# Optimization experiments

Measured on AMD Instinct MI355X. Metric: run time of the kernel, lower is better.

## Reference

```python
import jax, jax.numpy as jnp
import numpy as np

D_MODEL = 1024
NUM_HEADS = 16
HEAD_DIM = D_MODEL // NUM_HEADS
B, S = 2, 2048


def setup_inputs() -> dict:
    key = jax.random.key(0)
    ks = jax.random.split(key, 8)
    scale = 1.0 / np.sqrt(D_MODEL)
    inp = {
        "query": jax.random.normal(ks[0], (B, S, D_MODEL), jnp.float32),
        "key": jax.random.normal(ks[1], (B, S, D_MODEL), jnp.float32),
        "value": jax.random.normal(ks[2], (B, S, D_MODEL), jnp.float32),
        # causal mask, broadcastable over batch and heads
        "mask": jnp.tril(jnp.ones((S, S), dtype=bool))[None, None, :, :],
        # torch nn.Linear weights: y = x @ W.T (+ b)
        "Wq": jax.random.normal(ks[3], (D_MODEL, D_MODEL), jnp.float32) * scale,
        "Wk": jax.random.normal(ks[4], (D_MODEL, D_MODEL), jnp.float32) * scale,
        "Wv": jax.random.normal(ks[5], (D_MODEL, D_MODEL), jnp.float32) * scale,
        "Wo": jax.random.normal(ks[6], (D_MODEL, D_MODEL), jnp.float32) * scale,
        "bo": jax.random.normal(ks[7], (D_MODEL,), jnp.float32) * scale,
    }
    return inp


def _split_heads(x):
    b, s, _ = x.shape
    return x.reshape(b, s, NUM_HEADS, HEAD_DIM).transpose(0, 2, 1, 3)  # [B,H,S,Dh]


def reference(query, key, value, mask, Wq, Wk, Wv, Wo, bo):
    q = _split_heads(query @ Wq.T)
    k = _split_heads(key @ Wk.T)
    v = _split_heads(value @ Wv.T)
    scores = jnp.einsum("bhqd,bhkd->bhqk", q, k) / jnp.sqrt(jnp.float32(HEAD_DIM))
    scores = jnp.where(mask, scores, jnp.float32(-jnp.inf))
    attn = jax.nn.softmax(scores, axis=-1)
    out = jnp.einsum("bhqk,bhkd->bhqd", attn, v)  # [B,H,S,Dh]
    out = out.transpose(0, 2, 1, 3).reshape(query.shape[0], q.shape[2], D_MODEL)
    return out @ Wo.T + bo
```

## Files before the change

kernel.cpp:

```cpp
#include <hip/hip_runtime.h>
#include <hip/hip_bf16.h>

#define DM   1024
#define NH   16
#define HD   64
#define SEQ  2048
#define BATCH 2
#define MTOT (BATCH*SEQ)

typedef unsigned short u16;
typedef __attribute__((ext_vector_type(8))) short bf16x8;
typedef __attribute__((ext_vector_type(4))) float f32x4;

#define SC2F 0.1803368801111464f

__device__ __forceinline__ float bf2f(u16 h) {
  union { unsigned int i; float f; } u; u.i = ((unsigned int)h) << 16; return u.f;
}
__device__ __forceinline__ u16 f2bf(float f) {
  union { float f; unsigned int i; } u; u.f = f;
  unsigned int r = u.i + 0x7fffu + ((u.i >> 16) & 1u);
  return (u16)(r >> 16);
}
__device__ __forceinline__ unsigned int pk2(float lo, float hi) {
  union { float f; unsigned int u; } a, b; a.f = lo; b.f = hi;
  return ((a.u + 0x8000u) >> 16) | ((b.u + 0x8000u) & 0xFFFF0000u);
}
__device__ __forceinline__ unsigned int cvtpk(float lo, float hi) {
  unsigned int r;
  asm("v_cvt_pk_bf16_f32 %0, %1, %2" : "=v"(r) : "v"(lo), "v"(hi));
  return r;
}

__device__ __forceinline__ uint4 load8_bf16(const void* base, size_t elemOff, bool isf32) {
  if (!isf32) return *(const uint4*)((const u16*)base + elemOff);
  const float* f = (const float*)base + elemOff;
  f32x4 a = *(const f32x4*)f;
  f32x4 b = *(const f32x4*)(f + 4);
  union { u16 h[8]; uint4 v; } r;
  r.h[0]=f2bf(a[0]); r.h[1]=f2bf(a[1]); r.h[2]=f2bf(a[2]); r.h[3]=f2bf(a[3]);
  r.h[4]=f2bf(b[0]); r.h[5]=f2bf(b[1]); r.h[6]=f2bf(b[2]); r.h[7]=f2bf(b[3]);
  return r.v;
}

__global__ __launch_bounds__(256) void prep(
    const void* __restrict__ q, const void* __restrict__ k, const void* __restrict__ v,
    const void* __restrict__ wq, const void* __restrict__ wk, const void* __restrict__ wv,
    const void* __restrict__ wo, const void* __restrict__ bo,
    u16* __restrict__ Xq, u16* __restrict__ Xk, u16* __restrict__ Xv,
    u16* __restrict__ Wqb, u16* __restrict__ Wkb, u16* __restrict__ Wvb, u16* __restrict__ Wob,
    float* __restrict__ biasf, int* __restrict__ flag_out)
{
  const int tid = threadIdx.x;
  __shared__ int cnts[4];
  {
    const u16* qs = (const u16*)q;
    int e0 = (qs[tid*2]   >> 7) & 0xFF;
    int e1 = (qs[tid*2+1] >> 7) & 0xFF;
    int c = ((e0 >= 0x6E && e0 <= 0x8F) ? 1 : 0) + ((e1 >= 0x6E && e1 <= 0x8F) ? 1 : 0);
    c += __shfl_xor(c, 1);  c += __shfl_xor(c, 2);  c += __shfl_xor(c, 4);
    c += __shfl_xor(c, 8);  c += __shfl_xor(c, 16); c += __shfl_xor(c, 32);
    if ((tid & 63) == 0) cnts[tid >> 6] = c;
  }
  __syncthreads();
  const bool isf32 = (cnts[0] + cnts[1] + cnts[2] + cnts[3]) < 400;

  const int z = blockIdx.z;
  if (z == 7) {
    if (blockIdx.x == 0) {
      if (tid == 0) *flag_out = isf32 ? 0 : 1;
      for (int i = tid; i < DM; i += 256)
        biasf[i] = isf32 ? ((const float*)bo)[i] : bf2f(((const u16*)bo)[i]);
    }
    return;
  }
  const void* src; u16* dst; size_t n;
  switch (z) {
    case 0: src=q;  dst=Xq;  n=(size_t)MTOT*DM; break;
    case 1: src=k;  dst=Xk;  n=(size_t)MTOT*DM; break;
    case 2: src=v;  dst=Xv;  n=(size_t)MTOT*DM; break;
    case 3: src=wq; dst=Wqb; n=(size_t)DM*DM;   break;
    case 4: src=wk; dst=Wkb; n=(size_t)DM*DM;   break;
    case 5: src=wv; dst=Wvb; n=(size_t)DM*DM;   break;
    default: src=wo; dst=Wob; n=(size_t)DM*DM;  break;
  }
  const size_t stride = (size_t)gridDim.x * 256 * 8;
  for (size_t i = ((size_t)blockIdx.x * 256 + tid) * 8; i < n; i += stride)
    *(uint4*)(dst + i) = load8_bf16(src, i, isf32);
}

__device__ __forceinline__ void gld16(const u16* g, u16* l) {
  __builtin_amdgcn_global_load_lds(
      (const __attribute__((address_space(1))) void*)g,
      (__attribute__((address_space(3))) void*)l, 16, 0, 0);
}

__global__ __launch_bounds__(256) void gemm_qkv(
    const u16* __restrict__ X0, const u16* __restrict__ X1, const u16* __restrict__ X2,
    const u16* __restrict__ W0, const u16* __restrict__ W1, const u16* __restrict__ W2,
    u16* __restrict__ F0, u16* __restrict__ F1, u16* __restrict__ F2)
{
  __shared__ __align__(16) u16 smem[24576];
  u16* const A0 = smem;
  u16* const A1 = smem + 4096;
  u16* const A2 = smem + 8192;
  u16* const B0 = smem + 12288;
  u16* const B1 = smem + 16384;
  u16* const B2 = smem + 20480;

  const int zz = blockIdx.z;
  const u16* X = (zz==0) ? X0 : ((zz==1) ? X1 : X2);
  const u16* W = (zz==0) ? W0 : ((zz==1) ? W1 : W2);
  u16* outF    = (zz==0) ? F0 : ((zz==1) ? F1 : F2);

  const int tid = threadIdx.x;
  const int wave = tid >> 6, lane = tid & 63, quad = lane >> 4, l16 = lane & 15;
  const int wr = wave >> 1, wc = wave & 1;
  const int m0 = blockIdx.x * 128, n0 = blockIdx.y * 128;

  const int sg = ((lane & 3) ^ ((lane >> 3) & 3)) * 8;
  const int rS = wave*32 + (lane >> 2);
  const u16* gA0 = X + (size_t)(m0 + rS)*DM + sg;
  const u16* gA1 = X + (size_t)(m0 + rS + 16)*DM + sg;
  const u16* gB0 = W + (size_t)(n0 + rS)*DM + sg;
  const u16* gB1 = W + (size_t)(n0 + rS + 16)*DM + sg;
  const int so = wave*1024;

  const int xslot8 = (quad ^ ((l16 >> 1) & 3)) * 8;

  f32x4 acc[4][4];
#pragma unroll
  for (int i = 0; i < 4; i++)
#pragma unroll
    for (int j = 0; j < 4; j++) { acc[i][j][0]=0.f; acc[i][j][1]=0.f; acc[i][j][2]=0.f; acc[i][j][3]=0.f; }

  gld16(gA0, A0 + so);
  gld16(gA1, A0 + so + 512);
  gld16(gB0, B0 + so);
  gld16(gB1, B0 + so + 512);
  gld16(gA0 + 32, A1 + so);
  gld16(gA1 + 32, A1 + so + 512);
  gld16(gB0 + 32, B1 + so);
  gld16(gB1 + 32, B1 + so + 512);
  asm volatile("" ::: "memory");

  int cur = 0;
  for (int k0 = 0; k0 < DM; k0 += 32) {
    u16* const Ab = (cur == 0) ? A0 : ((cur == 1) ? A1 : A2);
    u16* const Bb = (cur == 0) ? B0 : ((cur == 1) ? B1 : B2);
    const int nxt = (cur == 2) ? 0 : cur + 1;
    const int nx2 = (nxt == 2) ? 0 : nxt + 1;
    if (k0 + 64 < DM) {
      u16* const An = (nx2 == 0) ? A0 : ((nx2 == 1) ? A1 : A2);
      u16* const Bn = (nx2 == 0) ? B0 : ((nx2 == 1) ? B1 : B2);
      gld16(gA0 + k0 + 64, An + so);
      gld16(gA1 + k0 + 64, An + so + 512);
      gld16(gB0 + k0 + 64, Bn + so);
      gld16(gB1 + k0 + 64, Bn + so + 512);
      asm volatile("s_waitcnt vmcnt(8)" ::: "memory");
    } else if (k0 + 32 < DM) {
      asm volatile("s_waitcnt vmcnt(4)" ::: "memory");
    } else {
      asm volatile("s_waitcnt vmcnt(0)" ::: "memory");
    }
    __builtin_amdgcn_s_barrier();
    asm volatile("" ::: "memory");

    bf16x8 af[4], bfr[4];
#pragma unroll
    for (int fr = 0; fr < 4; fr++)
      af[fr] = *(const bf16x8*)&Ab[(wr*64 + fr*16 + l16)*32 + xslot8];
#pragma unroll
    for (int fc = 0; fc < 4; fc++)
      bfr[fc] = *(const bf16x8*)&Bb[(wc*64 + fc*16 + l16)*32 + xslot8];
#pragma unroll
    for (int fr = 0; fr < 4; fr++)
#pragma unroll
      for (int fc = 0; fc < 4; fc++)
        acc[fr][fc] = __builtin_amdgcn_mfma_f32_16x16x32_bf16(af[fr], bfr[fc], acc[fr][fc], 0, 0, 0);

    asm volatile("" ::: "memory");
    __builtin_amdgcn_s_barrier();
    asm volatile("" ::: "memory");
    cur = nxt;
  }

  if (zz == 2) {
    u16* const Ts = smem;
    const int bb = m0 >> 11;
    const int s0 = m0 & (SEQ-1);
#pragma unroll
    for (int p = 0; p < 2; p++) {
      __syncthreads();
      if (wc == p) {
#pragma unroll
        for (int fr = 0; fr < 4; fr++) {
#pragma unroll
          for (int fc = 0; fc < 4; fc++) {
            const int dl = fc*16 + l16;
            const int sb = wr*64 + fr*16 + quad*4;
            const int slot = (sb >> 3) ^ (dl & 15);
            u16* rowp = &Ts[dl*128 + slot*8 + (sb & 7)];
            *(unsigned int*)(rowp)     = pk2(acc[fr][fc][0], acc[fr][fc][1]);
            *(unsigned int*)(rowp + 2) = pk2(acc[fr][fc][2], acc[fr][fc][3]);
          }
        }
      }
      __syncthreads();
      const int dl2 = tid >> 2, ch4 = tid & 3;
      const int hh = (n0 + p*64) >> 6;
      u16* dst = outF + ((size_t)(bb*NH + hh)*HD + dl2)*SEQ + s0 + ch4*32;
#pragma unroll
      for (int j = 0; j < 4; j++) {
        const int c  = ch4*4 + j;
        const int lo = (c >> 2)*32 + (c & 3)*4;
        const int hi = lo + 16;
        uint2 lo2 = *(const uint2*)&Ts[dl2*128 + (((lo >> 3) ^ (dl2 & 15))*8) + (lo & 7)];
        uint2 hi2 = *(const uint2*)&Ts[dl2*128 + (((hi >> 3) ^ (dl2 & 15))*8) + (hi & 7)];
        uint4 o; o.x = lo2.x; o.y = lo2.y; o.z = hi2.x; o.w = hi2.y;
        *(uint4*)&dst[j*8] = o;
      }
    }
    return;
  }

#pragma unroll
  for (int fr = 0; fr < 4; fr++) {
#pragma unroll
    for (int rr = 0; rr < 4; rr++) {
      const int m = m0 + wr*64 + fr*16 + quad*4 + rr;
#pragma unroll
      for (int fc = 0; fc < 4; fc++) {
        const int n = n0 + wc*64 + fc*16 + l16;
        float vv = acc[fr][fc][rr];
        if (zz == 0) vv *= SC2F;
        const int b = m >> 11, s = m & (SEQ-1), h = n >> 6, d = n & (HD-1);
        outF[((size_t)(b*NH + h)*SEQ + s)*HD + d] = f2bf(vv);
      }
    }
  }
}

__global__ __launch_bounds__(256) void gemm_out(
    const u16* __restrict__ X, const u16* __restrict__ W,
    const float* __restrict__ biasf, void* __restrict__ outP,
    const int* __restrict__ dflag)
{
  __shared__ __align__(16) u16 smem[18432];
  u16* const A0 = smem;
  u16* const A1 = smem + 4096;
  u16* const A2 = smem + 8192;
  u16* const B0 = smem + 12288;
  u16* const B1 = smem + 14336;
  u16* const B2 = smem + 16384;

  const int tid = threadIdx.x;
  const int wave = tid >> 6, lane = tid & 63, quad = lane >> 4, l16 = lane & 15;
  const int wr = wave >> 1, wc = wave & 1;
  const int m0 = blockIdx.x * 128, n0 = blockIdx.y * 64;

  const int sg = ((lane & 3) ^ ((lane >> 3) & 3)) * 8;
  const int rA = wave*32 + (lane >> 2);
  const int rB = wave*16 + (lane >> 2);
  const u16* gA0 = X + (size_t)(m0 + rA)*DM + sg;
  const u16* gA1 = X + (size_t)(m0 + rA + 16)*DM + sg;
  const u16* gB0 = W + (size_t)(n0 + rB)*DM + sg;
  const int soA = wave*1024, soB = wave*512;

  const int xslot8 = (quad ^ ((l16 >> 1) & 3)) * 8;

  f32x4 acc[4][2];
#pragma unroll
  for (int i = 0; i < 4; i++)
#pragma unroll
    for (int j = 0; j < 2; j++) { acc[i][j][0]=0.f; acc[i][j][1]=0.f; acc[i][j][2]=0.f; acc[i][j][3]=0.f; }

  gld16(gA0, A0 + soA);
  gld16(gA1, A0 + soA + 512);
  gld16(gB0, B0 + soB);
  gld16(gA0 + 32, A1 + soA);
  gld16(gA1 + 32, A1 + soA + 512);
  gld16(gB0 + 32, B1 + soB);
  asm volatile("" ::: "memory");

  int cur = 0;
  for (int k0 = 0; k0 < DM; k0 += 32) {
    u16* const Ab = (cur == 0) ? A0 : ((cur == 1) ? A1 : A2);
    u16* const Bb = (cur == 0) ? B0 : ((cur == 1) ? B1 : B2);
    const int nxt = (cur == 2) ? 0 : cur + 1;
    const int nx2 = (nxt == 2) ? 0 : nxt + 1;
    if (k0 + 64 < DM) {
      u16* const An = (nx2 == 0) ? A0 : ((nx2 == 1) ? A1 : A2);
      u16* const Bn = (nx2 == 0) ? B0 : ((nx2 == 1) ? B1 : B2);
      gld16(gA0 + k0 + 64, An + soA);
      gld16(gA1 + k0 + 64, An + soA + 512);
      gld16(gB0 + k0 + 64, Bn + soB);
      asm volatile("s_waitcnt vmcnt(6)" ::: "memory");
    } else if (k0 + 32 < DM) {
      asm volatile("s_waitcnt vmcnt(3)" ::: "memory");
    } else {
      asm volatile("s_waitcnt vmcnt(0)" ::: "memory");
    }
    __builtin_amdgcn_s_barrier();
    asm volatile("" ::: "memory");

    bf16x8 af[4], bfr[2];
#pragma unroll
    for (int fr = 0; fr < 4; fr++)
      af[fr] = *(const bf16x8*)&Ab[(wr*64 + fr*16 + l16)*32 + xslot8];
#pragma unroll
    for (int fc = 0; fc < 2; fc++)
      bfr[fc] = *(const bf16x8*)&Bb[(wc*32 + fc*16 + l16)*32 + xslot8];
#pragma unroll
    for (int fr = 0; fr < 4; fr++)
#pragma unroll
      for (int fc = 0; fc < 2; fc++)
        acc[fr][fc] = __builtin_amdgcn_mfma_f32_16x16x32_bf16(af[fr], bfr[fc], acc[fr][fc], 0, 0, 0);

    asm volatile("" ::: "memory");
    __builtin_amdgcn_s_barrier();
    asm volatile("" ::: "memory");
    cur = nxt;
  }

  const bool isf32 = (*dflag == 0);
#pragma unroll
  for (int fr = 0; fr < 4; fr++) {
#pragma unroll
    for (int rr = 0; rr < 4; rr++) {
      const int m = m0 + wr*64 + fr*16 + quad*4 + rr;
#pragma unroll
      for (int fc = 0; fc < 2; fc++) {
        const int n = n0 + wc*32 + fc*16 + l16;
        float vv = acc[fr][fc][rr] + biasf[n];
        if (isf32) ((float*)outP)[(size_t)m*DM + n] = vv;
        else       ((u16*)outP)[(size_t)m*DM + n]   = f2bf(vv);
      }
    }
  }
}

__global__ __launch_bounds__(256) void attn_mfma(
    const u16* __restrict__ Qb, const u16* __restrict__ Kb,
    const u16* __restrict__ Vtb,
    u16* __restrict__ aO)
{
  __shared__ u16 Ks[2][64*64];
  __shared__ u16 Vs[2][64*64];

  const int bh = blockIdx.x;
  const int py = blockIdx.y;
  int qt;
  if      (py < 8)  qt = 31 - py;
  else if (py < 16) qt = py - 8;
  else if (py < 24) qt = 39 - py;
  else              qt = py - 16;

  const u16* Qp = Qb  + (size_t)bh * SEQ * HD;
  const u16* Kp = Kb  + (size_t)bh * SEQ * HD;
  const u16* Vp = Vtb + (size_t)bh * HD * SEQ;

  const int tid  = threadIdx.x;
  const int wave = tid >> 6, lane = tid & 63, quad = lane >> 4, l16 = lane & 15;

  const int i0 = wave*128 + lane, i1 = i0 + 64;
  const int r0 = i0 >> 3, c0 = (i0 & 7) ^ (r0 & 7);
  const int r1 = i1 >> 3, c1 = (i1 & 7) ^ (r1 & 7);
  const int kq_off0 = r0*HD + c0*8;
  const int kq_off1 = r1*HD + c1*8;
  const int v_off0  = r0*SEQ + c0*8;
  const int v_off1  = r1*SEQ + c1*8;

  const int l7 = l16 & 7;
  const int ql = wave*16 + l16;
  const int so = wave*1024;

  const int khi = qt + 1;
  const int qg = qt*64 + ql;

  const u16* qrow = Qp + (size_t)qg * HD;
  const bf16x8 bq0 = *(const bf16x8*)(qrow + quad*8);
  const bf16x8 bq1 = *(const bf16x8*)(qrow + 32 + quad*8);

  f32x4 O[4];
#pragma unroll
  for (int u = 0; u < 4; u++) { O[u][0]=0.f; O[u][1]=0.f; O[u][2]=0.f; O[u][3]=0.f; }
  float mi = -3.0e38f;
  f32x4 lv = {0.f, 0.f, 0.f, 0.f};

  gld16(Kp + kq_off0, &Ks[0][so]);
  gld16(Kp + kq_off1, &Ks[0][so + 512]);
  gld16(Vp + v_off0, &Vs[0][so]);
  gld16(Vp + v_off1, &Vs[0][so + 512]);
  asm volatile("" ::: "memory");

  for (int kt = 0; kt < khi; kt++) {
    const int cb = kt & 1;
    const u16* kb = &Ks[cb][0];
    const u16* vb = &Vs[cb][0];
    if (kt + 1 < khi) {
      u16* kn = &Ks[cb ^ 1][so];
      u16* vn = &Vs[cb ^ 1][so];
      gld16(Kp + (kt+1)*(64*HD) + kq_off0, kn);
      gld16(Kp + (kt+1)*(64*HD) + kq_off1, kn + 512);
      gld16(Vp + (kt+1)*64 + v_off0, vn);
      gld16(Vp + (kt+1)*64 + v_off1, vn + 512);
      asm volatile("s_waitcnt vmcnt(4)" ::: "memory");
    } else {
      asm volatile("s_waitcnt vmcnt(0)" ::: "memory");
    }
    __builtin_amdgcn_s_barrier();
    asm volatile("" ::: "memory");

    f32x4 st[4];
#pragma unroll
    for (int t = 0; t < 4; t++) { st[t][0]=0.f; st[t][1]=0.f; st[t][2]=0.f; st[t][3]=0.f; }
#pragma unroll
    for (int s = 0; s < 2; s++) {
      const bf16x8 bq = s ? bq1 : bq0;
      const int ch = s*4 + quad;
#pragma unroll
      for (int t = 0; t < 4; t++) {
        bf16x8 ak = *(const bf16x8*)&kb[((t*16 + l16)*8 + (ch ^ l7))*8];
        st[t] = __builtin_amdgcn_mfma_f32_16x16x32_bf16(ak, bq, st[t], 0, 0, 0);
      }
    }

    if (kt == qt) {
#pragma unroll
      for (int t = 0; t < 4; t++)
#pragma unroll
        for (int r = 0; r < 4; r++)
          if (kt*64 + t*16 + quad*4 + r > qg) st[t][r] = -__builtin_inff();
    }

    f32x4 e0, e1, e2, e3;
    {
      const f32x4 miv = {mi, mi, mi, mi};
      f32x4 d0 = st[0] - miv, d1 = st[1] - miv, d2 = st[2] - miv, d3 = st[3] - miv;
      e0[0]=exp2f(d0[0]); e0[1]=exp2f(d0[1]); e0[2]=exp2f(d0[2]); e0[3]=exp2f(d0[3]);
      e1[0]=exp2f(d1[0]); e1[1]=exp2f(d1[1]); e1[2]=exp2f(d1[2]); e1[3]=exp2f(d1[3]);
      e2[0]=exp2f(d2[0]); e2[1]=exp2f(d2[1]); e2[2]=exp2f(d2[2]); e2[3]=exp2f(d2[3]);
      e3[0]=exp2f(d3[0]); e3[1]=exp2f(d3[1]); e3[2]=exp2f(d3[2]); e3[3]=exp2f(d3[3]);
    }
    f32x4 x01 = __builtin_elementwise_max(e0, e1);
    f32x4 x23 = __builtin_elementwise_max(e2, e3);
    f32x4 xm  = __builtin_elementwise_max(x01, x23);
    float em = fmaxf(fmaxf(xm[0], xm[1]), fmaxf(xm[2], xm[3]));
    if (__any(em > 256.0f)) {
      f32x4 m01 = __builtin_elementwise_max(st[0], st[1]);
      f32x4 m23 = __builtin_elementwise_max(st[2], st[3]);
      f32x4 mm  = __builtin_elementwise_max(m01, m23);
      float mx = fmaxf(fmaxf(mm[0], mm[1]), fmaxf(mm[2], mm[3]));
      mx = fmaxf(mx, __shfl_xor(mx, 16));
      mx = fmaxf(mx, __shfl_xor(mx, 32));
      const float nm = fmaxf(mi, mx);
      const float al = exp2f(mi - nm);
      mi = nm;
      const f32x4 alv = {al, al, al, al};
      lv *= alv;
      O[0] *= alv; O[1] *= alv; O[2] *= alv; O[3] *= alv;
      const f32x4 miv = {mi, mi, mi, mi};
      f32x4 d0 = st[0] - miv, d1 = st[1] - miv, d2 = st[2] - miv, d3 = st[3] - miv;
      e0[0]=exp2f(d0[0]); e0[1]=exp2f(d0[1]); e0[2]=exp2f(d0[2]); e0[3]=exp2f(d0[3]);
      e1[0]=exp2f(d1[0]); e1[1]=exp2f(d1[1]); e1[2]=exp2f(d1[2]); e1[3]=exp2f(d1[3]);
      e2[0]=exp2f(d2[0]); e2[1]=exp2f(d2[1]); e2[2]=exp2f(d2[2]); e2[3]=exp2f(d2[3]);
      e3[0]=exp2f(d3[0]); e3[1]=exp2f(d3[1]); e3[2]=exp2f(d3[2]); e3[3]=exp2f(d3[3]);
    }

    unsigned int w[4][2];
    w[0][0] = cvtpk(e0[0], e0[1]); w[0][1] = cvtpk(e0[2], e0[3]);
    w[1][0] = cvtpk(e1[0], e1[1]); w[1][1] = cvtpk(e1[2], e1[3]);
    w[2][0] = cvtpk(e2[0], e2[1]); w[2][1] = cvtpk(e2[2], e2[3]);
    w[3][0] = cvtpk(e3[0], e3[1]); w[3][1] = cvtpk(e3[2], e3[3]);
    lv += (e0 + e1) + (e2 + e3);

#pragma unroll
    for (int s = 0; s < 2; s++) {
      union { unsigned int u[4]; bf16x8 v; } bp;
      bp.u[0] = w[2*s][0];   bp.u[1] = w[2*s][1];
      bp.u[2] = w[2*s+1][0]; bp.u[3] = w[2*s+1][1];
      const int ch = s*4 + quad;
#pragma unroll
      for (int u = 0; u < 4; u++) {
        bf16x8 av = *(const bf16x8*)&vb[((u*16 + l16)*8 + (ch ^ l7))*8];
        O[u] = __builtin_amdgcn_mfma_f32_16x16x32_bf16(av, bp.v, O[u], 0, 0, 0);
      }
    }

    asm volatile("" ::: "memory");
    __builtin_amdgcn_s_barrier();
    asm volatile("" ::: "memory");
  }

  float ls = (lv[0] + lv[1]) + (lv[2] + lv[3]);
  ls += __shfl_xor(ls, 16);
  ls += __shfl_xor(ls, 32);
  const float inv = 1.0f / ls;

  const int b = bh >> 4, h = bh & 15;
  u16* outp = aO + ((size_t)(b*SEQ + qt*64 + ql))*DM + h*HD;
#pragma unroll
  for (int u = 0; u < 4; u++) {
    uint2 u2;
    u2.x = pk2(O[u][0]*inv, O[u][1]*inv);
    u2.y = pk2(O[u][2]*inv, O[u][3]*inv);
    *(uint2*)&outp[u*16 + quad*4] = u2;
  }
}

extern "C" void kernel_launch(void* const* d_in, const int* in_sizes, int n_in,
                              void* d_out, int out_size, void* d_ws, size_t ws_size,
                              hipStream_t stream) {
  const void* q  = d_in[0];
  const void* k  = d_in[1];
  const void* v  = d_in[2];
  const void* wq = d_in[4];
  const void* wk = d_in[5];
  const void* wv = d_in[6];
  const void* wo = d_in[7];
  const void* bo = d_in[8];

  const size_t TX = (size_t)MTOT*DM;
  const size_t TW = (size_t)DM*DM;
  u16* ws  = (u16*)d_ws;
  u16* Xq  = ws;
  u16* Xk  = ws + TX;
  u16* Xv  = ws + 2*TX;
  u16* Wqb = ws + 3*TX;
  u16* Wkb = Wqb + TW;
  u16* Wvb = Wqb + 2*TW;
  u16* Wob = Wqb + 3*TW;
  u16* Qw  = ws + 3*TX + 4*TW;
  u16* Kw  = Qw + TX;
  u16* Vt  = Qw + 2*TX;
  u16*   aO     = Xq;
  float* biasf  = (float*)(Qw + 3*TX);
  int*   fl     = (int*)(biasf + DM);

  dim3 blk(256);
  prep<<<dim3(512, 1, 8), blk, 0, stream>>>(q, k, v, wq, wk, wv, wo, bo,
      Xq, Xk, Xv, Wqb, Wkb, Wvb, Wob, biasf, fl);
  gemm_qkv<<<dim3(MTOT/128, DM/128, 3), blk, 0, stream>>>(
      Xq, Xk, Xv, Wqb, Wkb, Wvb, Qw, Kw, Vt);
  attn_mfma<<<dim3(BATCH*NH, 32, 1), blk, 0, stream>>>(Qw, Kw, Vt, aO);
  gemm_out<<<dim3(MTOT/128, DM/64), blk, 0, stream>>>(aO, Wob, biasf, d_out, fl);
}
```

Baseline: 217.9 us.

## Asymmetric prefetch: triple-buffer A, double-buffer B, one barrier per k-step

Both GEMM kernels now keep A tiles triple-buffered (prefetched two steps ahead) but B tiles only double-buffered (one step ahead). This cuts LDS use. The pre-compute wait and barrier are removed, leaving a single waitcnt plus barrier at the end of each iteration, which halves the barriers in the k-loop. The risk is that B loads have less latency slack, and the waitcnt counts must exactly match the outstanding loads to stay correct.

```diff
diff --git a/kernel.cpp b/kernel.cpp
--- a/kernel.cpp
+++ b/kernel.cpp
@@ -100,13 +100,12 @@
     const u16* __restrict__ W0, const u16* __restrict__ W1, const u16* __restrict__ W2,
     u16* __restrict__ F0, u16* __restrict__ F1, u16* __restrict__ F2)
 {
-  __shared__ __align__(16) u16 smem[24576];
+  __shared__ __align__(16) u16 smem[20480];
   u16* const A0 = smem;
   u16* const A1 = smem + 4096;
   u16* const A2 = smem + 8192;
-  u16* const B0 = smem + 12288;
-  u16* const B1 = smem + 16384;
-  u16* const B2 = smem + 20480;
+  u16* const Bb0 = smem + 12288;
+  u16* const Bb1 = smem + 16384;
 
   const int zz = blockIdx.z;
   const u16* X = (zz==0) ? X0 : ((zz==1) ? X1 : X2);
@@ -136,34 +135,32 @@
 
   gld16(gA0, A0 + so);
   gld16(gA1, A0 + so + 512);
-  gld16(gB0, B0 + so);
-  gld16(gB1, B0 + so + 512);
+  gld16(gB0, Bb0 + so);
+  gld16(gB1, Bb0 + so + 512);
   gld16(gA0 + 32, A1 + so);
   gld16(gA1 + 32, A1 + so + 512);
-  gld16(gB0 + 32, B1 + so);
-  gld16(gB1 + 32, B1 + so + 512);
+  asm volatile("s_waitcnt vmcnt(2)" ::: "memory");
+  __builtin_amdgcn_s_barrier();
   asm volatile("" ::: "memory");
 
-  int cur = 0;
+  int curA = 0, curB = 0;
   for (int k0 = 0; k0 < DM; k0 += 32) {
-    u16* const Ab = (cur == 0) ? A0 : ((cur == 1) ? A1 : A2);
-    u16* const Bb = (cur == 0) ? B0 : ((cur == 1) ? B1 : B2);
-    const int nxt = (cur == 2) ? 0 : cur + 1;
-    const int nx2 = (nxt == 2) ? 0 : nxt + 1;
-    if (k0 + 64 < DM) {
-      u16* const An = (nx2 == 0) ? A0 : ((nx2 == 1) ? A1 : A2);
-      u16* const Bn = (nx2 == 0) ? B0 : ((nx2 == 1) ? B1 : B2);
+    u16* const Ab = (curA == 0) ? A0 : ((curA == 1) ? A1 : A2);
+    u16* const Bb = curB ? Bb1 : Bb0;
+    const bool m1 = (k0 + 32 < DM);
+    const bool m2 = (k0 + 64 < DM);
+
+    if (m1) {
+      u16* const Bn = curB ? Bb0 : Bb1;
+      gld16(gB0 + k0 + 32, Bn + so);
+      gld16(gB1 + k0 + 32, Bn + so + 512);
+    }
+    if (m2) {
+      const int a2 = (curA >= 1) ? curA - 1 : curA + 2;
+      u16* const An = (a2 == 0) ? A0 : ((a2 == 1) ? A1 : A2);
       gld16(gA0 + k0 + 64, An + so);
       gld16(gA1 + k0 + 64, An + so + 512);
-      gld16(gB0 + k0 + 64, Bn + so);
-      gld16(gB1 + k0 + 64, Bn + so + 512);
-      asm volatile("s_waitcnt vmcnt(8)" ::: "memory");
-    } else if (k0 + 32 < DM) {
-      asm volatile("s_waitcnt vmcnt(4)" ::: "memory");
-    } else {
-      asm volatile("s_waitcnt vmcnt(0)" ::: "memory");
-    }
-    __builtin_amdgcn_s_barrier();
+    }
     asm volatile("" ::: "memory");
 
     bf16x8 af[4], bfr[4];
@@ -179,10 +176,12 @@
       for (int fc = 0; fc < 4; fc++)
         acc[fr][fc] = __builtin_amdgcn_mfma_f32_16x16x32_bf16(af[fr], bfr[fc], acc[fr][fc], 0, 0, 0);
 
-    asm volatile("" ::: "memory");
+    if (m2)      { asm volatile("s_waitcnt vmcnt(2)" ::: "memory"); }
+    else if (m1) { asm volatile("s_waitcnt vmcnt(0)" ::: "memory"); }
     __builtin_amdgcn_s_barrier();
     asm volatile("" ::: "memory");
-    cur = nxt;
+    curA = (curA == 2) ? 0 : curA + 1;
+    curB ^= 1;
   }
 
   if (zz == 2) {
@@ -246,13 +245,12 @@
     const float* __restrict__ biasf, void* __restrict__ outP,
     const int* __restrict__ dflag)
 {
-  __shared__ __align__(16) u16 smem[18432];
+  __shared__ __align__(16) u16 smem[16384];
   u16* const A0 = smem;
   u16* const A1 = smem + 4096;
   u16* const A2 = smem + 8192;
-  u16* const B0 = smem + 12288;
-  u16* const B1 = smem + 14336;
-  u16* const B2 = smem + 16384;
+  u16* const Bb0 = smem + 12288;
+  u16* const Bb1 = smem + 14336;
 
   const int tid = threadIdx.x;
   const int wave = tid >> 6, lane = tid & 63, quad = lane >> 4, l16 = lane & 15;
@@ -277,31 +275,30 @@
 
   gld16(gA0, A0 + soA);
   gld16(gA1, A0 + soA + 512);
-  gld16(gB0, B0 + soB);
+  gld16(gB0, Bb0 + soB);
   gld16(gA0 + 32, A1 + soA);
   gld16(gA1 + 32, A1 + soA + 512);
-  gld16(gB0 + 32, B1 + soB);
+  asm volatile("s_waitcnt vmcnt(2)" ::: "memory");
+  __builtin_amdgcn_s_barrier();
   asm volatile("" ::: "memory");
 
-  int cur = 0;
+  int curA = 0, curB = 0;
   for (int k0 = 0; k0 < DM; k0 += 32) {
-    u16* const Ab = (cur == 0) ? A0 : ((cur == 1) ? A1 : A2);
-    u16* const Bb = (cur == 0) ? B0 : ((cur == 1) ? B1 : B2);
-    const int nxt = (cur == 2) ? 0 : cur + 1;
-    const int nx2 = (nxt == 2) ? 0 : nxt + 1;
-    if (k0 + 64 < DM) {
-      u16* const An = (nx2 == 0) ? A0 : ((nx2 == 1) ? A1 : A2);
-      u16* const Bn = (nx2 == 0) ? B0 : ((nx2 == 1) ? B1 : B2);
+    u16* const Ab = (curA == 0) ? A0 : ((curA == 1) ? A1 : A2);
+    u16* const Bb = curB ? Bb1 : Bb0;
+    const bool m1 = (k0 + 32 < DM);
+    const bool m2 = (k0 + 64 < DM);
+
+    if (m1) {
+      u16* const Bn = curB ? Bb0 : Bb1;
+      gld16(gB0 + k0 + 32, Bn + soB);
+    }
+    if (m2) {
+      const int a2 = (curA >= 1) ? curA - 1 : curA + 2;
+      u16* const An = (a2 == 0) ? A0 : ((a2 == 1) ? A1 : A2);
       gld16(gA0 + k0 + 64, An + soA);
       gld16(gA1 + k0 + 64, An + soA + 512);
-      gld16(gB0 + k0 + 64, Bn + soB);
-      asm volatile("s_waitcnt vmcnt(6)" ::: "memory");
-    } else if (k0 + 32 < DM) {
-      asm volatile("s_waitcnt vmcnt(3)" ::: "memory");
-    } else {
-      asm volatile("s_waitcnt vmcnt(0)" ::: "memory");
-    }
-    __builtin_amdgcn_s_barrier();
+    }
     asm volatile("" ::: "memory");
 
     bf16x8 af[4], bfr[2];
@@ -317,10 +314,12 @@
       for (int fc = 0; fc < 2; fc++)
         acc[fr][fc] = __builtin_amdgcn_mfma_f32_16x16x32_bf16(af[fr], bfr[fc], acc[fr][fc], 0, 0, 0);
 
-    asm volatile("" ::: "memory");
+    if (m2)      { asm volatile("s_waitcnt vmcnt(2)" ::: "memory"); }
+    else if (m1) { asm volatile("s_waitcnt vmcnt(0)" ::: "memory"); }
     __builtin_amdgcn_s_barrier();
     asm volatile("" ::: "memory");
-    cur = nxt;
+    curA = (curA == 2) ? 0 : curA + 1;
+    curB ^= 1;
   }
 
   const bool isf32 = (*dflag == 0);
```

Result: slower. 222.7 us (+2.2%).
